# Performance work log

Measured on AMD Instinct MI355X. Metric: run time of the kernel, lower is better.

## Reference

```python
import jax, jax.numpy as jnp
import numpy as np

EPS_MEAN = 1e-10


def setup_inputs() -> dict:
    key = jax.random.key(0)
    ks = jax.random.split(key, 16)
    B, N, F, D = 2, 512, 128, 3
    s = lambda fan_in: 1.0 / np.sqrt(fan_in)
    return {
        "h": jax.random.normal(ks[0], (B, N, F), jnp.float32),
        "coord": jax.random.normal(ks[1], (B, N, D), jnp.float32),
        "mask": jnp.ones((B, N), jnp.float32),
        "edge_w1": jax.random.normal(ks[2], (2 * F + 1, F), jnp.float32) * s(2 * F + 1),
        "edge_b1": jnp.zeros((F,), jnp.float32),
        "edge_w2": jax.random.normal(ks[3], (F, F), jnp.float32) * s(F),
        "edge_b2": jnp.zeros((F,), jnp.float32),
        "node_w1": jax.random.normal(ks[4], (2 * F, F), jnp.float32) * s(2 * F),
        "node_b1": jnp.zeros((F,), jnp.float32),
        "node_w2": jax.random.normal(ks[5], (F, F), jnp.float32) * s(F),
        "node_b2": jnp.zeros((F,), jnp.float32),
        "coord_w1": jax.random.normal(ks[6], (F, F), jnp.float32) * s(F),
        "coord_b1": jnp.zeros((F,), jnp.float32),
        # xavier_uniform with gain=0.001 -> tiny weights
        "coord_w2": jax.random.normal(ks[7], (F, 1), jnp.float32) * 0.001 * s(F),
    }


def reference(h, coord, mask, edge_w1, edge_b1, edge_w2, edge_b2,
              node_w1, node_b1, node_w2, node_b2,
              coord_w1, coord_b1, coord_w2):
    silu = jax.nn.silu
    B, N, F = h.shape
    # mask inputs
    h = h * mask[:, :, None]
    coord = coord * mask[:, :, None]
    mask2d = mask[:, :, None] * mask[:, None, :]            # [B,N,N]

    # coord2radial
    coord_diff = coord[:, :, None] - coord[:, None]          # [B,N,N,3]
    radial = jnp.sum(coord_diff ** 2, axis=-1, keepdims=True)  # [B,N,N,1]
    radial = radial * mask2d[..., None]
    coord_diff = coord_diff * mask2d[..., None]

    # edge model: source[b,i,j]=h[b,j], target[b,i,j]=h[b,i]
    source = jnp.broadcast_to(h[:, None, :, :], (B, N, N, F))
    target = jnp.broadcast_to(h[:, :, None, :], (B, N, N, F))
    edge_in = jnp.concatenate([source, target, radial], axis=-1)  # [B,N,N,2F+1]
    m = silu(edge_in @ edge_w1 + edge_b1)
    m = silu(m @ edge_w2 + edge_b2)                          # [B,N,N,F]
    m = m * mask2d[..., None]

    # coord model
    embed = silu(m @ coord_w1 + coord_b1) @ coord_w2         # [B,N,N,1]
    trans = coord_diff * embed * mask2d[..., None]           # [B,N,N,3]
    denom = jnp.sum(mask2d, axis=2, keepdims=True) + EPS_MEAN  # [B,N,1]
    coord_new = coord + jnp.sum(trans, axis=2) / denom
    coord_new = coord_new * mask[:, :, None]

    # node model
    agg = jnp.sum(m, axis=2)                                 # [B,N,F]
    node_in = jnp.concatenate([h, agg], axis=-1) * mask[:, :, None]
    out = silu(node_in @ node_w1 + node_b1) @ node_w2 + node_b2
    h_new = (h + out) * mask[:, :, None]

    return h_new, coord_new
```

## Files before the change

kernel.cpp:

```cpp
#include <hip/hip_runtime.h>

#define B_ 2
#define N_ 512
#define F_ 128
#define TJ 64
#define MSTRIDE 136

typedef __attribute__((ext_vector_type(8))) short short8;
typedef __attribute__((ext_vector_type(4))) float floatx4;

__device__ __forceinline__ float fsilu(float x) {
    float e = __expf(-x);
    return x * __builtin_amdgcn_rcpf(1.0f + e);
}
__device__ __forceinline__ unsigned pack2(float a, float b) {
    return __builtin_amdgcn_perm(__float_as_uint(b) + 0x8000u,
                                 __float_as_uint(a) + 0x8000u, 0x07060302u);
}

__global__ __launch_bounds__(256) void egcl_prep(
        const float* __restrict__ h, const float* __restrict__ mask,
        const float* __restrict__ ew1, const float* __restrict__ ew2,
        const float* __restrict__ cw1,
        float* __restrict__ Hs, float* __restrict__ Ht,
        unsigned short* __restrict__ W2P, unsigned short* __restrict__ WcP,
        float* __restrict__ msum) {
    __shared__ float sh[8][F_];
    const int blk = blockIdx.x, tid = threadIdx.x;
    if (blk < 128) {
        const int r0 = blk * 8;
        const int col = tid & 127, half = tid >> 7;
#pragma unroll
        for (int rr = 0; rr < 4; ++rr) {
            int row = rr * 2 + half;
            sh[row][col] = h[(r0 + row) * F_ + col] * mask[r0 + row];
        }
        __syncthreads();
        const float* W = ew1 + half * F_ * F_ + col;
        float acc[8] = {0.f, 0.f, 0.f, 0.f, 0.f, 0.f, 0.f, 0.f};
#pragma unroll 8
        for (int k = 0; k < F_; ++k) {
            float w = W[k * F_];
#pragma unroll
            for (int r = 0; r < 8; ++r) acc[r] += sh[r][k] * w;
        }
        float* dst = half ? Ht : Hs;
#pragma unroll
        for (int r = 0; r < 8; ++r) dst[(r0 + r) * F_ + col] = acc[r];
    } else if (blk < 144) {
        const int wsel = (blk - 128) >> 3;
        const int mt = (blk - 128) & 7;
        const float* src = wsel ? cw1 : ew2;
        unsigned short* dst = wsel ? WcP : W2P;
        const int ln = tid & 63, kk = tid >> 6;
        const int qq = ln >> 4, ll = ln & 15;
#pragma unroll
        for (int rep = 0; rep < 2; ++rep) {
            const int krow = kk * 32 + qq * 8 + rep * 4;
            float f0 = src[(krow + 0) * F_ + mt * 16 + ll];
            float f1 = src[(krow + 1) * F_ + mt * 16 + ll];
            float f2 = src[(krow + 2) * F_ + mt * 16 + ll];
            float f3 = src[(krow + 3) * F_ + mt * 16 + ll];
            uint2 u = make_uint2(pack2(f0, f1), pack2(f2, f3));
            *(uint2*)(dst + ((mt * 4 + kk) * 64 + ln) * 8 + rep * 4) = u;
        }
    } else {
        const int bb = blk - 144;
        float v = mask[bb * N_ + tid] + mask[bb * N_ + 256 + tid];
        v += __shfl_xor(v, 1);  v += __shfl_xor(v, 2);
        v += __shfl_xor(v, 4);  v += __shfl_xor(v, 8);
        v += __shfl_xor(v, 16); v += __shfl_xor(v, 32);
        const int wave = tid >> 6, lane = tid & 63;
        if (lane == 0) sh[0][wave] = v;
        __syncthreads();
        if (tid == 0) msum[bb] = sh[0][0] + sh[0][1] + sh[0][2] + sh[0][3];
    }
}

#define L_M1   0
#define L_M    17408
#define L_HB   34816
#define L_W1R  35328
#define L_EMBP 35840
#define L_AGG  44032
#define L_HIN  44544
#define L_AGGT 45056
#define L_TL   45568
#define L_NP   46080
#define L_F2S  47104
#define L_CSW  47360
#define L_TOTAL 47408

__global__ __launch_bounds__(256, 2) void egcl_main(
        const float* __restrict__ h, const float* __restrict__ coord,
        const float* __restrict__ mask,
        const float* __restrict__ eb1, const float* __restrict__ eb2,
        const float* __restrict__ cb1, const float* __restrict__ cw2,
        const float* __restrict__ nw1, const float* __restrict__ nb1,
        const float* __restrict__ nw2, const float* __restrict__ nb2,
        const float* __restrict__ ew1,
        const float* __restrict__ Hs, const float* __restrict__ Ht,
        const unsigned short* __restrict__ W2P,
        const unsigned short* __restrict__ WcP,
        const float* __restrict__ msum,
        float* __restrict__ out_h, float* __restrict__ out_coord) {
    extern __shared__ char smem[];
    unsigned short* m1s = (unsigned short*)(smem + L_M1);
    unsigned short* ms  = (unsigned short*)(smem + L_M);
    float* HB    = (float*)(smem + L_HB);
    float* W1R   = (float*)(smem + L_W1R);
    float* embp  = (float*)(smem + L_EMBP);
    float* aggs  = (float*)(smem + L_AGG);
    float* hin   = (float*)(smem + L_HIN);
    float* aggt  = (float*)(smem + L_AGGT);
    float* tl    = (float*)(smem + L_TL);
    float* np    = (float*)(smem + L_NP);
    float* f2s   = (float*)(smem + L_F2S);
    float* csw   = (float*)(smem + L_CSW);

    const int tid  = threadIdx.x;
    const int wave = tid >> 6, lane = tid & 63;
    const int q = lane >> 4, l15 = lane & 15;
    const int wg = wave;
    const int bi = blockIdx.x;
    const int b  = bi >> 9;
    const float mask_i = mask[bi];

    short8 w2f[2][4], wcf[2][4];
#pragma unroll
    for (int s = 0; s < 2; ++s)
#pragma unroll
        for (int kk = 0; kk < 4; ++kk) {
            w2f[s][kk] = *(const short8*)(W2P + (((2 * wg + s) * 4 + kk) * 64 + lane) * 8);
            wcf[s][kk] = *(const short8*)(WcP + (((2 * wg + s) * 4 + kk) * 64 + lane) * 8);
        }
    floatx4 e2b[2], c1b[2], w2c[2];
#pragma unroll
    for (int s = 0; s < 2; ++s) {
        e2b[s] = *(const floatx4*)(eb2 + wg * 32 + s * 16 + q * 4);
        c1b[s] = *(const floatx4*)(cb1 + wg * 32 + s * 16 + q * 4);
        w2c[s] = *(const floatx4*)(cw2 + wg * 32 + s * 16 + q * 4);
    }

    if (tid < F_) {
        HB[tid]  = Ht[bi * F_ + tid] + eb1[tid];
        W1R[tid] = ew1[2 * F_ * F_ + tid];
        hin[tid] = h[bi * F_ + tid] * mask_i;
    }
    const float cmi0 = coord[bi * 3 + 0] * mask_i;
    const float cmi1 = coord[bi * 3 + 1] * mask_i;
    const float cmi2 = coord[bi * 3 + 2] * mask_i;
    __syncthreads();

    const int kseg = tid & 15, jq = tid >> 4;
    float hbk[8], w1k[8];
    {
        const floatx4* hp = (const floatx4*)(HB + kseg * 8);
        const floatx4* wp = (const floatx4*)(W1R + kseg * 8);
        floatx4 a = hp[0], bb2 = hp[1], cc = wp[0], dd = wp[1];
#pragma unroll
        for (int t = 0; t < 4; ++t) {
            hbk[t] = a[t]; hbk[4 + t] = bb2[t];
            w1k[t] = cc[t]; w1k[4 + t] = dd[t];
        }
    }
    floatx4 agg0 = {0.f, 0.f, 0.f, 0.f}, agg1 = {0.f, 0.f, 0.f, 0.f};

    for (int p = 0; p < N_ / TJ; ++p) {
#pragma unroll
        for (int r = 0; r < 4; ++r) {
            int row = jq * 4 + r;
            int jg = b * N_ + p * TJ + row;
            float mj = mask[jg];
            float c0 = coord[jg * 3 + 0] * mj;
            float c1 = coord[jg * 3 + 1] * mj;
            float c2 = coord[jg * 3 + 2] * mj;
            float d0 = cmi0 - c0, d1 = cmi1 - c1, d2 = cmi2 - c2;
            float f2 = mask_i * mj;
            float rad = (d0 * d0 + d1 * d1 + d2 * d2) * f2;
            if (kseg == 0) f2s[row] = f2;
            const floatx4* hsp = (const floatx4*)(Hs + jg * F_ + kseg * 8);
            floatx4 h0 = hsp[0], h1 = hsp[1];
            float x[8];
#pragma unroll
            for (int t = 0; t < 4; ++t) {
                x[t]     = fsilu(h0[t] + hbk[t]     + rad * w1k[t]);
                x[4 + t] = fsilu(h1[t] + hbk[4 + t] + rad * w1k[4 + t]);
            }
            union { short8 s8; unsigned u[4]; } pu;
            pu.u[0] = pack2(x[0], x[1]); pu.u[1] = pack2(x[2], x[3]);
            pu.u[2] = pack2(x[4], x[5]); pu.u[3] = pack2(x[6], x[7]);
            *(short8*)(m1s + row * MSTRIDE + kseg * 8) = pu.s8;
        }
        __syncthreads();
#pragma unroll
        for (int jt = 0; jt < 4; ++jt) {
            const int jrow = jt * 16 + l15;
            const unsigned short* m1r = m1s + jrow * MSTRIDE;
            floatx4 a0 = e2b[0], a1 = e2b[1];
#pragma unroll
            for (int kk = 0; kk < 4; ++kk) {
                short8 bf = *(const short8*)(m1r + kk * 32 + q * 8);
                a0 = __builtin_amdgcn_mfma_f32_16x16x32_bf16(w2f[0][kk], bf, a0, 0, 0, 0);
                a1 = __builtin_amdgcn_mfma_f32_16x16x32_bf16(w2f[1][kk], bf, a1, 0, 0, 0);
            }
            const float f2 = f2s[jrow];
            float v0[4], v1[4];
#pragma unroll
            for (int rg = 0; rg < 4; ++rg) {
                v0[rg] = fsilu(a0[rg]) * f2;
                v1[rg] = fsilu(a1[rg]) * f2;
                agg0[rg] += v0[rg];
                agg1[rg] += v1[rg];
            }
            unsigned short* mr = ms + jrow * MSTRIDE + wg * 32 + q * 4;
            *(uint2*)(mr)      = make_uint2(pack2(v0[0], v0[1]), pack2(v0[2], v0[3]));
            *(uint2*)(mr + 16) = make_uint2(pack2(v1[0], v1[1]), pack2(v1[2], v1[3]));
        }
        __syncthreads();
#pragma unroll
        for (int jt = 0; jt < 4; ++jt) {
            const int jrow = jt * 16 + l15;
            const unsigned short* mr = ms + jrow * MSTRIDE;
            floatx4 a0 = c1b[0], a1 = c1b[1];
#pragma unroll
            for (int kk = 0; kk < 4; ++kk) {
                short8 bf = *(const short8*)(mr + kk * 32 + q * 8);
                a0 = __builtin_amdgcn_mfma_f32_16x16x32_bf16(wcf[0][kk], bf, a0, 0, 0, 0);
                a1 = __builtin_amdgcn_mfma_f32_16x16x32_bf16(wcf[1][kk], bf, a1, 0, 0, 0);
            }
            float es = 0.f;
#pragma unroll
            for (int rg = 0; rg < 4; ++rg) {
                es += fsilu(a0[rg]) * w2c[0][rg];
                es += fsilu(a1[rg]) * w2c[1][rg];
            }
            es += __shfl_xor(es, 16);
            es += __shfl_xor(es, 32);
            if (q == 0) embp[wg * 512 + p * TJ + jrow] = es;
        }
    }

    __syncthreads();

    float cs0 = 0.f, cs1 = 0.f, cs2 = 0.f;
#pragma unroll
    for (int jj = 0; jj < 2; ++jj) {
        int j = tid * 2 + jj;
        int jg = b * N_ + j;
        float e = embp[j] + embp[512 + j] + embp[1024 + j] + embp[1536 + j];
        float mj = mask[jg];
        float c0 = coord[jg * 3 + 0] * mj;
        float c1 = coord[jg * 3 + 1] * mj;
        float c2 = coord[jg * 3 + 2] * mj;
        float f2 = mask_i * mj;
        float w = e * f2 * f2;
        cs0 += (cmi0 - c0) * w;
        cs1 += (cmi1 - c1) * w;
        cs2 += (cmi2 - c2) * w;
    }
    cs0 += __shfl_xor(cs0, 1); cs0 += __shfl_xor(cs0, 2);
    cs0 += __shfl_xor(cs0, 4); cs0 += __shfl_xor(cs0, 8);
    cs0 += __shfl_xor(cs0, 16); cs0 += __shfl_xor(cs0, 32);
    cs1 += __shfl_xor(cs1, 1); cs1 += __shfl_xor(cs1, 2);
    cs1 += __shfl_xor(cs1, 4); cs1 += __shfl_xor(cs1, 8);
    cs1 += __shfl_xor(cs1, 16); cs1 += __shfl_xor(cs1, 32);
    cs2 += __shfl_xor(cs2, 1); cs2 += __shfl_xor(cs2, 2);
    cs2 += __shfl_xor(cs2, 4); cs2 += __shfl_xor(cs2, 8);
    cs2 += __shfl_xor(cs2, 16); cs2 += __shfl_xor(cs2, 32);
    if (lane == 0) {
        csw[wave * 3 + 0] = cs0;
        csw[wave * 3 + 1] = cs1;
        csw[wave * 3 + 2] = cs2;
    }

#pragma unroll
    for (int rg = 0; rg < 4; ++rg) {
        float v = agg0[rg];
        v += __shfl_xor(v, 1); v += __shfl_xor(v, 2);
        v += __shfl_xor(v, 4); v += __shfl_xor(v, 8);
        agg0[rg] = v;
        float u = agg1[rg];
        u += __shfl_xor(u, 1); u += __shfl_xor(u, 2);
        u += __shfl_xor(u, 4); u += __shfl_xor(u, 8);
        agg1[rg] = u;
    }
    if (l15 == 0) {
        *(floatx4*)(aggs + wg * 32 + q * 4)      = agg0;
        *(floatx4*)(aggs + wg * 32 + 16 + q * 4) = agg1;
    }
    __syncthreads();
    if (tid < F_) aggt[tid] = aggs[tid] * mask_i;
    __syncthreads();
    {
        int half = tid >> 7, col = tid & 127;
        const float* W = nw1 + half * 128 * F_ + col;
        float s = 0.f;
        if (half == 0) {
#pragma unroll 8
            for (int k = 0; k < F_; ++k) s += hin[k] * W[k * F_];
            s *= mask_i;
        } else {
#pragma unroll 8
            for (int k = 0; k < F_; ++k) s += aggt[k] * W[k * F_];
        }
        np[tid] = s;
    }
    __syncthreads();
    if (tid < F_) tl[tid] = fsilu(np[tid] + np[128 + tid] + nb1[tid]);
    __syncthreads();
    if (tid < F_) {
        float s = nb2[tid];
#pragma unroll 8
        for (int k = 0; k < F_; ++k) s += tl[k] * nw2[k * F_ + tid];
        out_h[bi * F_ + tid] = (hin[tid] + s) * mask_i;
    } else if (tid < F_ + 3) {
        int d = tid - F_;
        float cs = csw[d] + csw[3 + d] + csw[6 + d] + csw[9 + d];
        float denom = mask_i * msum[b] + 1e-10f;
        float cm = (d == 0) ? cmi0 : ((d == 1) ? cmi1 : cmi2);
        out_coord[bi * 3 + d] = (cm + cs * __builtin_amdgcn_rcpf(denom)) * mask_i;
    }
}

extern "C" void kernel_launch(void* const* d_in, const int* in_sizes, int n_in,
                              void* d_out, int out_size, void* d_ws, size_t ws_size,
                              hipStream_t stream) {
    const float* h     = (const float*)d_in[0];
    const float* coord = (const float*)d_in[1];
    const float* mask  = (const float*)d_in[2];
    const float* ew1   = (const float*)d_in[3];
    const float* eb1   = (const float*)d_in[4];
    const float* ew2   = (const float*)d_in[5];
    const float* eb2   = (const float*)d_in[6];
    const float* nw1   = (const float*)d_in[7];
    const float* nb1   = (const float*)d_in[8];
    const float* nw2   = (const float*)d_in[9];
    const float* nb2   = (const float*)d_in[10];
    const float* cw1   = (const float*)d_in[11];
    const float* cb1   = (const float*)d_in[12];
    const float* cw2   = (const float*)d_in[13];

    float* Hs = (float*)d_ws;
    float* Ht = Hs + B_ * N_ * F_;
    unsigned short* W2P = (unsigned short*)(Ht + B_ * N_ * F_);
    unsigned short* WcP = W2P + F_ * F_;
    float* msum = (float*)(WcP + F_ * F_);

    float* out_h = (float*)d_out;
    float* out_coord = out_h + B_ * N_ * F_;

    egcl_prep<<<146, 256, 0, stream>>>(h, mask, ew1, ew2, cw1,
                                       Hs, Ht, W2P, WcP, msum);
    egcl_main<<<B_ * N_, 256, L_TOTAL, stream>>>(
        h, coord, mask, eb1, eb2, cb1, cw2, nw1, nb1, nw2, nb2, ew1,
        Hs, Ht, W2P, WcP, msum, out_h, out_coord);
}
```

Baseline: 181.6 us.

## Double-buffer the edge-MLP LDS tiles and fuse the coordinate reduction into the pipeline

The j-tile loop is software-pipelined. The m1 and m LDS buffers are double-buffered, so the first-layer build for tile p+1 and the second GEMM for tile p-1 run alongside the first GEMM for tile p. This cuts the block barriers from two per tile to one. The per-j coordinate differences and mask product are kept in a ring buffer, so the coordinate update is accumulated directly inside the second GEMM. That replaces the separate embp store-and-reduce pass and its extra barrier. The cost is roughly 30 KB more LDS per block, which could limit occupancy at two blocks per CU.

After: 184.3 us. About the same (+1.5%).

```diff
diff --git a/kernel.cpp b/kernel.cpp
--- a/kernel.cpp
+++ b/kernel.cpp
@@ -78,18 +78,17 @@
 }
 
 #define L_M1   0
-#define L_M    17408
-#define L_HB   34816
-#define L_W1R  35328
-#define L_EMBP 35840
-#define L_AGG  44032
-#define L_HIN  44544
-#define L_AGGT 45056
-#define L_TL   45568
-#define L_NP   46080
-#define L_F2S  47104
-#define L_CSW  47360
-#define L_TOTAL 47408
+#define L_MS   34816
+#define L_HB   69632
+#define L_W1R  70144
+#define L_DJS  70656
+#define L_AGG  74752
+#define L_HIN  75264
+#define L_AGGT 75776
+#define L_TL   76288
+#define L_NP   76800
+#define L_CSW  77824
+#define L_TOTAL 77872
 
 __global__ __launch_bounds__(256, 2) void egcl_main(
         const float* __restrict__ h, const float* __restrict__ coord,
@@ -106,16 +105,15 @@
         float* __restrict__ out_h, float* __restrict__ out_coord) {
     extern __shared__ char smem[];
     unsigned short* m1s = (unsigned short*)(smem + L_M1);
-    unsigned short* ms  = (unsigned short*)(smem + L_M);
+    unsigned short* ms  = (unsigned short*)(smem + L_MS);
     float* HB    = (float*)(smem + L_HB);
     float* W1R   = (float*)(smem + L_W1R);
-    float* embp  = (float*)(smem + L_EMBP);
+    float* djs   = (float*)(smem + L_DJS);
     float* aggs  = (float*)(smem + L_AGG);
     float* hin   = (float*)(smem + L_HIN);
     float* aggt  = (float*)(smem + L_AGGT);
     float* tl    = (float*)(smem + L_TL);
     float* np    = (float*)(smem + L_NP);
-    float* f2s   = (float*)(smem + L_F2S);
     float* csw   = (float*)(smem + L_CSW);
 
     const int tid  = threadIdx.x;
@@ -165,12 +163,15 @@
         }
     }
     floatx4 agg0 = {0.f, 0.f, 0.f, 0.f}, agg1 = {0.f, 0.f, 0.f, 0.f};
-
-    for (int p = 0; p < N_ / TJ; ++p) {
+    float cs0 = 0.f, cs1 = 0.f, cs2 = 0.f;
+
+    auto m1build = [&](int pp) {
+        unsigned short* dst = m1s + (pp & 1) * (TJ * MSTRIDE);
+        float* dj = djs + (pp & 3) * (TJ * 4);
 #pragma unroll
         for (int r = 0; r < 4; ++r) {
             int row = jq * 4 + r;
-            int jg = b * N_ + p * TJ + row;
+            int jg = b * N_ + pp * TJ + row;
             float mj = mask[jg];
             float c0 = coord[jg * 3 + 0] * mj;
             float c1 = coord[jg * 3 + 1] * mj;
@@ -178,7 +179,10 @@
             float d0 = cmi0 - c0, d1 = cmi1 - c1, d2 = cmi2 - c2;
             float f2 = mask_i * mj;
             float rad = (d0 * d0 + d1 * d1 + d2 * d2) * f2;
-            if (kseg == 0) f2s[row] = f2;
+            if (kseg == 0) {
+                floatx4 v = {d0, d1, d2, f2};
+                *(floatx4*)(dj + row * 4) = v;
+            }
             const floatx4* hsp = (const floatx4*)(Hs + jg * F_ + kseg * 8);
             floatx4 h0 = hsp[0], h1 = hsp[1];
             float x[8];
@@ -190,13 +194,18 @@
             union { short8 s8; unsigned u[4]; } pu;
             pu.u[0] = pack2(x[0], x[1]); pu.u[1] = pack2(x[2], x[3]);
             pu.u[2] = pack2(x[4], x[5]); pu.u[3] = pack2(x[6], x[7]);
-            *(short8*)(m1s + row * MSTRIDE + kseg * 8) = pu.s8;
-        }
-        __syncthreads();
+            *(short8*)(dst + row * MSTRIDE + kseg * 8) = pu.s8;
+        }
+    };
+
+    auto gemm1 = [&](int p) {
+        const unsigned short* m1b = m1s + (p & 1) * (TJ * MSTRIDE);
+        unsigned short* msb = ms + (p & 1) * (TJ * MSTRIDE);
+        const float* djp = djs + (p & 3) * (TJ * 4);
 #pragma unroll
         for (int jt = 0; jt < 4; ++jt) {
             const int jrow = jt * 16 + l15;
-            const unsigned short* m1r = m1s + jrow * MSTRIDE;
+            const unsigned short* m1r = m1b + jrow * MSTRIDE;
             floatx4 a0 = e2b[0], a1 = e2b[1];
 #pragma unroll
             for (int kk = 0; kk < 4; ++kk) {
@@ -204,7 +213,7 @@
                 a0 = __builtin_amdgcn_mfma_f32_16x16x32_bf16(w2f[0][kk], bf, a0, 0, 0, 0);
                 a1 = __builtin_amdgcn_mfma_f32_16x16x32_bf16(w2f[1][kk], bf, a1, 0, 0, 0);
             }
-            const float f2 = f2s[jrow];
+            const float f2 = djp[jrow * 4 + 3];
             float v0[4], v1[4];
 #pragma unroll
             for (int rg = 0; rg < 4; ++rg) {
@@ -213,15 +222,19 @@
                 agg0[rg] += v0[rg];
                 agg1[rg] += v1[rg];
             }
-            unsigned short* mr = ms + jrow * MSTRIDE + wg * 32 + q * 4;
+            unsigned short* mr = msb + jrow * MSTRIDE + wg * 32 + q * 4;
             *(uint2*)(mr)      = make_uint2(pack2(v0[0], v0[1]), pack2(v0[2], v0[3]));
             *(uint2*)(mr + 16) = make_uint2(pack2(v1[0], v1[1]), pack2(v1[2], v1[3]));
         }
-        __syncthreads();
+    };
+
+    auto gemm2 = [&](int p) {
+        const unsigned short* msb = ms + (p & 1) * (TJ * MSTRIDE);
+        const float* djp = djs + (p & 3) * (TJ * 4);
 #pragma unroll
         for (int jt = 0; jt < 4; ++jt) {
             const int jrow = jt * 16 + l15;
-            const unsigned short* mr = ms + jrow * MSTRIDE;
+            const unsigned short* mr = msb + jrow * MSTRIDE;
             floatx4 a0 = c1b[0], a1 = c1b[1];
 #pragma unroll
             for (int kk = 0; kk < 4; ++kk) {
@@ -235,30 +248,24 @@
                 es += fsilu(a0[rg]) * w2c[0][rg];
                 es += fsilu(a1[rg]) * w2c[1][rg];
             }
-            es += __shfl_xor(es, 16);
-            es += __shfl_xor(es, 32);
-            if (q == 0) embp[wg * 512 + p * TJ + jrow] = es;
-        }
-    }
-
-    __syncthreads();
-
-    float cs0 = 0.f, cs1 = 0.f, cs2 = 0.f;
-#pragma unroll
-    for (int jj = 0; jj < 2; ++jj) {
-        int j = tid * 2 + jj;
-        int jg = b * N_ + j;
-        float e = embp[j] + embp[512 + j] + embp[1024 + j] + embp[1536 + j];
-        float mj = mask[jg];
-        float c0 = coord[jg * 3 + 0] * mj;
-        float c1 = coord[jg * 3 + 1] * mj;
-        float c2 = coord[jg * 3 + 2] * mj;
-        float f2 = mask_i * mj;
-        float w = e * f2 * f2;
-        cs0 += (cmi0 - c0) * w;
-        cs1 += (cmi1 - c1) * w;
-        cs2 += (cmi2 - c2) * w;
-    }
+            floatx4 dj4 = *(const floatx4*)(djp + jrow * 4);
+            float w = es * dj4[3] * dj4[3];
+            cs0 += dj4[0] * w;
+            cs1 += dj4[1] * w;
+            cs2 += dj4[2] * w;
+        }
+    };
+
+    m1build(0);
+    __syncthreads();
+    for (int p = 0; p < N_ / TJ; ++p) {
+        if (p > 0) gemm2(p - 1);
+        gemm1(p);
+        if (p < N_ / TJ - 1) m1build(p + 1);
+        __syncthreads();
+    }
+    gemm2(N_ / TJ - 1);
+
     cs0 += __shfl_xor(cs0, 1); cs0 += __shfl_xor(cs0, 2);
     cs0 += __shfl_xor(cs0, 4); cs0 += __shfl_xor(cs0, 8);
     cs0 += __shfl_xor(cs0, 16); cs0 += __shfl_xor(cs0, 32);
@@ -273,7 +280,6 @@
         csw[wave * 3 + 1] = cs1;
         csw[wave * 3 + 2] = cs2;
     }
-
 #pragma unroll
     for (int rg = 0; rg < 4; ++rg) {
         float v = agg0[rg];
```
